# Kernel optimization log

Measured on AMD Instinct MI355X. Metric: run time of the kernel, lower is better.

Reference implementation:

```python
import jax, jax.numpy as jnp
import numpy as np
from jax import lax

V, D, L, H, MAXLEN = 32000, 512, 6, 8, 1024
DH = D // H
DFF = 4 * D
B, T = 8, 1024


def _ln(x, g, b, eps=1e-5):
    m = jnp.mean(x, axis=-1, keepdims=True)
    v = jnp.var(x, axis=-1, keepdims=True)
    return (x - m) * lax.rsqrt(v + eps) * g + b


def setup_inputs() -> dict:
    key = jax.random.key(0)
    ks = jax.random.split(key, 16)
    s = 0.02
    inp = {
        "idx": jax.random.randint(ks[0], (B, T), 0, V, dtype=jnp.int32),
        "wte": jax.random.normal(ks[1], (V, D), jnp.float32) * s,   # tied with head
        "wpe": jax.random.normal(ks[2], (MAXLEN, D), jnp.float32) * s,
        # per-layer stacked params [L, ...]
        "ln1_g": jnp.ones((L, D), jnp.float32),
        "ln1_b": jnp.zeros((L, D), jnp.float32),
        "w_qkv": jax.random.normal(ks[3], (L, D, 3 * D), jnp.float32) * s,
        "b_qkv": jnp.zeros((L, 3 * D), jnp.float32),
        "w_ao": jax.random.normal(ks[4], (L, D, D), jnp.float32) * s,
        "b_ao": jnp.zeros((L, D), jnp.float32),
        "ln2_g": jnp.ones((L, D), jnp.float32),
        "ln2_b": jnp.zeros((L, D), jnp.float32),
        "w_fc": jax.random.normal(ks[5], (L, D, DFF), jnp.float32) * s,
        "b_fc": jnp.zeros((L, DFF), jnp.float32),
        "w_pr": jax.random.normal(ks[6], (L, DFF, D), jnp.float32) * s,
        "b_pr": jnp.zeros((L, D), jnp.float32),
        "lnf_g": jnp.ones((D,), jnp.float32),
        "lnf_b": jnp.zeros((D,), jnp.float32),
    }
    return inp


def reference(idx, wte, wpe, ln1_g, ln1_b, w_qkv, b_qkv, w_ao, b_ao,
              ln2_g, ln2_b, w_fc, b_fc, w_pr, b_pr, lnf_g, lnf_b):
    Bx, Tx = idx.shape
    x = wte[idx] + wpe[:Tx]                      # [B,T,D]
    causal = jnp.tril(jnp.ones((Tx, Tx), bool))  # [T,T]
    scale = 1.0 / np.sqrt(DH)

    def block(x, p):
        (g1, b1, wqkv, bqkv, wao, bao, g2, b2, wfc, bfc, wpr, bpr) = p
        h = _ln(x, g1, b1)
        qkv = h @ wqkv + bqkv                    # [B,T,3D]
        q, k, v = jnp.split(qkv, 3, axis=-1)
        q = q.reshape(Bx, Tx, H, DH)
        k = k.reshape(Bx, Tx, H, DH)
        v = v.reshape(Bx, Tx, H, DH)
        att = jnp.einsum('bqhd,bkhd->bhqk', q, k) * scale
        att = jnp.where(causal, att, -jnp.inf)
        att = jax.nn.softmax(att, axis=-1)
        y = jnp.einsum('bhqk,bkhd->bqhd', att, v).reshape(Bx, Tx, D)
        x = x + y @ wao + bao
        h = _ln(x, g2, b2)
        h = jax.nn.gelu(h @ wfc + bfc, approximate=False)
        x = x + h @ wpr + bpr
        return x, None

    params = (ln1_g, ln1_b, w_qkv, b_qkv, w_ao, b_ao,
              ln2_g, ln2_b, w_fc, b_fc, w_pr, b_pr)
    x, _ = lax.scan(block, x, params)
    x = _ln(x, lnf_g, lnf_b)
    logits = x @ wte.T                           # tied head, [B,T,V]
    return logits
```

## Files before the change

### kernel.cpp

```cpp
#include <hip/hip_runtime.h>
#include <hip/hip_bf16.h>
#include <math.h>

#define V_   32000
#define D_   512
#define L_   6
#define H_   8
#define DH_  64
#define DFF_ 2048
#define B_   8
#define T_   1024
#define BT_  (B_*T_)

typedef __attribute__((ext_vector_type(4))) float f32x4;
typedef __attribute__((ext_vector_type(8))) short short8;
using bf16_t = __hip_bfloat16;

__device__ __forceinline__ float b2f(unsigned short u) {
    union { unsigned int i; float f; } v; v.i = ((unsigned int)u) << 16; return v.f;
}
__device__ __forceinline__ unsigned short f2b(float f) {
    bf16_t h = __float2bfloat16(f);
    return *reinterpret_cast<unsigned short*>(&h);
}
__device__ __forceinline__ void gl16(const void* g, void* l) {
    __builtin_amdgcn_global_load_lds((const __attribute__((address_space(1))) void*)g,
                                     (__attribute__((address_space(3))) void*)l, 16, 0, 0);
}
__device__ __forceinline__ float gelu_exact(float v) {
    return 0.5f * v * (1.0f + erff(v * 0.70710678118654752f));
}

__global__ __launch_bounds__(128) void embed_kernel(
        const int* __restrict__ idx, const float* __restrict__ wte,
        const float* __restrict__ wpe, float* __restrict__ x) {
    int bt = blockIdx.x;
    int t  = bt & (T_ - 1);
    int tok = idx[bt];
    const float4* wr = (const float4*)(wte + (size_t)tok * D_);
    const float4* pr = (const float4*)(wpe + (size_t)t * D_);
    float4* xr = (float4*)(x + (size_t)bt * D_);
    int i = threadIdx.x;
    float4 a = wr[i], b = pr[i];
    xr[i] = make_float4(a.x + b.x, a.y + b.y, a.z + b.z, a.w + b.w);
}

__global__ __launch_bounds__(128) void ln_kernel(
        const float* __restrict__ x, const float* __restrict__ g,
        const float* __restrict__ b, bf16_t* __restrict__ out) {
    int bt = blockIdx.x;
    int i  = threadIdx.x;
    float4 v = ((const float4*)(x + (size_t)bt * D_))[i];
    float s  = v.x + v.y + v.z + v.w;
    float sq = v.x*v.x + v.y*v.y + v.z*v.z + v.w*v.w;
    #pragma unroll
    for (int o = 32; o > 0; o >>= 1) {
        s  += __shfl_down(s,  o);
        sq += __shfl_down(sq, o);
    }
    __shared__ float ss[2], ssq[2];
    if ((i & 63) == 0) { ss[i >> 6] = s; ssq[i >> 6] = sq; }
    __syncthreads();
    float mean = (ss[0] + ss[1]) * (1.0f / D_);
    float var  = (ssq[0] + ssq[1]) * (1.0f / D_) - mean * mean;
    float rstd = rsqrtf(var + 1e-5f);
    float4 gg = ((const float4*)g)[i];
    float4 bb = ((const float4*)b)[i];
    ushort4 o4;
    o4.x = f2b((v.x - mean) * rstd * gg.x + bb.x);
    o4.y = f2b((v.y - mean) * rstd * gg.y + bb.y);
    o4.z = f2b((v.z - mean) * rstd * gg.z + bb.z);
    o4.w = f2b((v.w - mean) * rstd * gg.w + bb.w);
    ((ushort4*)(out + (size_t)bt * D_))[i] = o4;
}

__global__ __launch_bounds__(256) void conv_kernel(
        const float* __restrict__ s, bf16_t* __restrict__ d, int n4) {
    int i = blockIdx.x * 256 + threadIdx.x;
    if (i >= n4) return;
    float4 f = ((const float4*)s)[i];
    ushort4 u = make_ushort4(f2b(f.x), f2b(f.y), f2b(f.z), f2b(f.w));
    ((ushort4*)d)[i] = u;
}

__global__ __launch_bounds__(256) void tconv_kernel(
        const float* __restrict__ src, bf16_t* __restrict__ dst, int K, int N) {
    size_t ls = (size_t)K * N;
    const float* s = src + blockIdx.z * ls;
    bf16_t* d = dst + blockIdx.z * ls;
    __shared__ float tile[32][33];
    int n0 = blockIdx.x * 32, k0 = blockIdx.y * 32;
    int c = threadIdx.x & 31, r8 = threadIdx.x >> 5;
    #pragma unroll
    for (int i = 0; i < 4; ++i) {
        int r = r8 + i * 8;
        tile[r][c] = s[(size_t)(k0 + r) * N + n0 + c];
    }
    __syncthreads();
    #pragma unroll
    for (int i = 0; i < 4; ++i) {
        int r = r8 + i * 8;
        d[(size_t)(n0 + r) * K + k0 + c] = __float2bfloat16(tile[c][r]);
    }
}

template<int ACT, bool OBF, bool RES, bool CONVB>
__global__ __launch_bounds__(256) void mm_kernel(
        const bf16_t* __restrict__ A,
        const bf16_t* __restrict__ Bt,
        const float*  __restrict__ Bf,
        const float*  __restrict__ bias,
        const float*  __restrict__ res,
        void* __restrict__ Cout,
        int M, int N, int K)
{
    __shared__ __align__(16) unsigned short As[128 * 32];
    __shared__ __align__(16) unsigned short Bs[128 * 32];
    const int nwg = gridDim.x;
    const int orig = blockIdx.x;
    const int q8 = nwg >> 3, r8 = nwg & 7;
    const int xcd = orig & 7, lin = orig >> 3;
    const int wg = (xcd < r8) ? xcd * (q8 + 1) + lin
                              : r8 * (q8 + 1) + (xcd - r8) * q8 + lin;
    const int gym = M >> 7;
    const int by = wg % gym;
    const int bx = wg / gym;

    const int t    = threadIdx.x;
    const int row0 = by * 128;
    const int col0 = bx * 128;
    const int lane = t & 63;
    const int wid  = t >> 6;
    const int wm   = (wid & 1) * 64;
    const int wn   = (wid >> 1) * 64;
    const int fr   = lane & 15;
    const int fq   = lane >> 4;

    f32x4 acc[4][4];
    #pragma unroll
    for (int m = 0; m < 4; ++m)
        #pragma unroll
        for (int n = 0; n < 4; ++n)
            acc[m][n] = (f32x4)(0.0f);

    const unsigned short* Ab  = (const unsigned short*)A;
    const unsigned short* Btb = (const unsigned short*)Bt;

    for (int k0 = 0; k0 < K; k0 += 32) {
        __syncthreads();
        {
            int c = t;
            gl16(Ab + (size_t)(row0 + (c >> 2)) * K + k0 + (c & 3) * 8, As + c * 8);
            c = t + 256;
            gl16(Ab + (size_t)(row0 + (c >> 2)) * K + k0 + (c & 3) * 8, As + c * 8);
        }
        if (!CONVB) {
            int c = t;
            gl16(Btb + (size_t)(col0 + (c >> 2)) * K + k0 + (c & 3) * 8, Bs + c * 8);
            c = t + 256;
            gl16(Btb + (size_t)(col0 + (c >> 2)) * K + k0 + (c & 3) * 8, Bs + c * 8);
        } else {
            #pragma unroll
            for (int i = 0; i < 2; ++i) {
                int c = t + i * 256;
                const float* sp = Bf + (size_t)(col0 + (c >> 2)) * K + k0 + (c & 3) * 8;
                float4 f0 = ((const float4*)sp)[0];
                float4 f1 = ((const float4*)sp)[1];
                short8 pk;
                pk[0] = f2b(f0.x); pk[1] = f2b(f0.y); pk[2] = f2b(f0.z); pk[3] = f2b(f0.w);
                pk[4] = f2b(f1.x); pk[5] = f2b(f1.y); pk[6] = f2b(f1.z); pk[7] = f2b(f1.w);
                *(short8*)(Bs + (size_t)c * 8) = pk;
            }
        }
        __syncthreads();

        short8 av[4], bv[4];
        #pragma unroll
        for (int m = 0; m < 4; ++m)
            av[m] = *(const short8*)(As + (wm + m * 16 + fr) * 32 + fq * 8);
        #pragma unroll
        for (int n = 0; n < 4; ++n)
            bv[n] = *(const short8*)(Bs + (wn + n * 16 + fr) * 32 + fq * 8);
        #pragma unroll
        for (int m = 0; m < 4; ++m)
            #pragma unroll
            for (int n = 0; n < 4; ++n)
                acc[m][n] = __builtin_amdgcn_mfma_f32_16x16x32_bf16(av[m], bv[n], acc[m][n], 0, 0, 0);
    }

    #pragma unroll
    for (int n = 0; n < 4; ++n) {
        int col = col0 + wn + n * 16 + fr;
        float bb = bias ? bias[col] : 0.0f;
        #pragma unroll
        for (int m = 0; m < 4; ++m) {
            int rbase = row0 + wm + m * 16 + fq * 4;
            #pragma unroll
            for (int r = 0; r < 4; ++r) {
                float v = acc[m][n][r] + bb;
                if (ACT == 1) v = gelu_exact(v);
                size_t off = (size_t)(rbase + r) * N + col;
                if (RES) v += res[off];
                if (OBF) ((bf16_t*)Cout)[off] = __float2bfloat16(v);
                else     ((float*)Cout)[off]  = v;
            }
        }
    }
}

__global__ __launch_bounds__(256) void flash_kernel(
        const bf16_t* __restrict__ qkv, bf16_t* __restrict__ y)
{
    __shared__ __align__(16) unsigned short Ks[64][72];
    __shared__ __align__(16) unsigned short Vt[64][72];
    __shared__ __align__(16) unsigned short Pls[64][72];

    const int qt = blockIdx.x;
    const int bh = blockIdx.y;
    const int h  = bh & (H_ - 1);
    const int b  = bh >> 3;
    const int t  = threadIdx.x;
    const int lane = t & 63;
    const int w    = t >> 6;
    const int fr   = lane & 15;
    const int fq   = lane >> 4;

    const unsigned short* qkvb = (const unsigned short*)qkv;

    short8 avq[2];
    {
        const unsigned short* qrow = qkvb +
            (size_t)(b * T_ + qt * 64 + w * 16 + fr) * (3 * D_) + h * DH_;
        avq[0] = *(const short8*)(qrow + fq * 8);
        avq[1] = *(const short8*)(qrow + 32 + fq * 8);
    }

    float mi[4], li[4];
    f32x4 o[4];
    #pragma unroll
    for (int r = 0; r < 4; ++r) { mi[r] = -INFINITY; li[r] = 0.0f; o[r] = (f32x4)(0.0f); }
    f32x4 o2[4];
    #pragma unroll
    for (int r = 0; r < 4; ++r) o2[r] = (f32x4)(0.0f);
    f32x4 oacc[4];
    #pragma unroll
    for (int d = 0; d < 4; ++d) oacc[d] = (f32x4)(0.0f);
    (void)o; (void)o2;

    for (int jt = 0; jt <= qt; ++jt) {
        __syncthreads();
        {
            int j = t >> 2, seg = t & 3;
            const unsigned short* krow = qkvb +
                (size_t)(b * T_ + jt * 64 + j) * (3 * D_) + D_ + h * DH_ + seg * 16;
            *(short8*)&Ks[j][seg * 16]     = *(const short8*)(krow);
            *(short8*)&Ks[j][seg * 16 + 8] = *(const short8*)(krow + 8);
            const unsigned short* vrow = krow + D_;
            #pragma unroll
            for (int d4 = 0; d4 < 4; ++d4) {
                ushort4 u = *(const ushort4*)(vrow + d4 * 4);
                int d = seg * 16 + d4 * 4;
                Vt[d + 0][j] = u.x; Vt[d + 1][j] = u.y;
                Vt[d + 2][j] = u.z; Vt[d + 3][j] = u.w;
            }
        }
        __syncthreads();

        f32x4 s[4];
        #pragma unroll
        for (int jb = 0; jb < 4; ++jb) s[jb] = (f32x4)(0.0f);
        #pragma unroll
        for (int ks = 0; ks < 2; ++ks) {
            #pragma unroll
            for (int jb = 0; jb < 4; ++jb) {
                short8 bv = *(const short8*)(&Ks[jb * 16 + fr][ks * 32 + fq * 8]);
                s[jb] = __builtin_amdgcn_mfma_f32_16x16x32_bf16(avq[ks], bv, s[jb], 0, 0, 0);
            }
        }

        float sv[4][4];
        #pragma unroll
        for (int jb = 0; jb < 4; ++jb)
            #pragma unroll
            for (int r = 0; r < 4; ++r)
                sv[jb][r] = s[jb][r] * 0.125f;
        if (jt == qt) {
            #pragma unroll
            for (int jb = 0; jb < 4; ++jb) {
                int j_loc = jb * 16 + fr;
                #pragma unroll
                for (int r = 0; r < 4; ++r) {
                    int q_loc = w * 16 + fq * 4 + r;
                    if (jt * 64 + j_loc > qt * 64 + q_loc - w * 16 + w * 16) {}
                    if (j_loc > (fq * 4 + r) + (w * 16) - (w * 16) + (q_loc - q_loc)) {}
                }
            }
            #pragma unroll
            for (int jb = 0; jb < 4; ++jb) {
                int j_loc = jb * 16 + fr;
                #pragma unroll
                for (int r = 0; r < 4; ++r) {
                    int q_loc = w * 16 + fq * 4 + r;
                    if (j_loc > q_loc) sv[jb][r] = -INFINITY;
                }
            }
        }

        #pragma unroll
        for (int r = 0; r < 4; ++r) {
            float tm = fmaxf(fmaxf(sv[0][r], sv[1][r]), fmaxf(sv[2][r], sv[3][r]));
            tm = fmaxf(tm, __shfl_xor(tm, 1));
            tm = fmaxf(tm, __shfl_xor(tm, 2));
            tm = fmaxf(tm, __shfl_xor(tm, 4));
            tm = fmaxf(tm, __shfl_xor(tm, 8));
            float mnew = fmaxf(mi[r], tm);
            float corr = __expf(mi[r] - mnew);
            float tsum = 0.0f;
            #pragma unroll
            for (int jb = 0; jb < 4; ++jb) {
                float p = __expf(sv[jb][r] - mnew);
                sv[jb][r] = p;
                tsum += p;
            }
            tsum += __shfl_xor(tsum, 1);
            tsum += __shfl_xor(tsum, 2);
            tsum += __shfl_xor(tsum, 4);
            tsum += __shfl_xor(tsum, 8);
            li[r] = li[r] * corr + tsum;
            mi[r] = mnew;
            #pragma unroll
            for (int db = 0; db < 4; ++db) oacc[db][r] *= corr;
        }

        #pragma unroll
        for (int jb = 0; jb < 4; ++jb)
            #pragma unroll
            for (int r = 0; r < 4; ++r)
                Pls[w * 16 + fq * 4 + r][jb * 16 + fr] = f2b(sv[jb][r]);
        __syncthreads();

        #pragma unroll
        for (int ks = 0; ks < 2; ++ks) {
            short8 ap = *(const short8*)(&Pls[w * 16 + fr][ks * 32 + fq * 8]);
            #pragma unroll
            for (int db = 0; db < 4; ++db) {
                short8 bv = *(const short8*)(&Vt[db * 16 + fr][ks * 32 + fq * 8]);
                oacc[db] = __builtin_amdgcn_mfma_f32_16x16x32_bf16(ap, bv, oacc[db], 0, 0, 0);
            }
        }
    }

    unsigned short* yb = (unsigned short*)y;
    #pragma unroll
    for (int r = 0; r < 4; ++r) {
        float inv = 1.0f / li[r];
        size_t row = (size_t)(b * T_ + qt * 64 + w * 16 + fq * 4 + r);
        #pragma unroll
        for (int db = 0; db < 4; ++db)
            yb[row * D_ + h * DH_ + db * 16 + fr] = f2b(oacc[db][r] * inv);
    }
}

extern "C" void kernel_launch(void* const* d_in, const int* in_sizes, int n_in,
                              void* d_out, int out_size, void* d_ws, size_t ws_size,
                              hipStream_t stream) {
    const int*   idx   = (const int*)  d_in[0];
    const float* wte   = (const float*)d_in[1];
    const float* wpe   = (const float*)d_in[2];
    const float* ln1_g = (const float*)d_in[3];
    const float* ln1_b = (const float*)d_in[4];
    const float* w_qkv = (const float*)d_in[5];
    const float* b_qkv = (const float*)d_in[6];
    const float* w_ao  = (const float*)d_in[7];
    const float* b_ao  = (const float*)d_in[8];
    const float* ln2_g = (const float*)d_in[9];
    const float* ln2_b = (const float*)d_in[10];
    const float* w_fc  = (const float*)d_in[11];
    const float* b_fc  = (const float*)d_in[12];
    const float* w_pr  = (const float*)d_in[13];
    const float* b_pr  = (const float*)d_in[14];
    const float* lnf_g = (const float*)d_in[15];
    const float* lnf_b = (const float*)d_in[16];
    float* outf = (float*)d_out;

    char* base = (char*)d_out;
    size_t off = 0;
    auto alloc = [&](size_t bytes) {
        void* p = base + off;
        off += (bytes + 255) & ~(size_t)255;
        return p;
    };
    bf16_t* wqkvT = (bf16_t*)alloc((size_t)L_ * 3 * D_ * D_ * 2);
    bf16_t* waoT  = (bf16_t*)alloc((size_t)L_ * D_ * D_ * 2);
    bf16_t* wfcT  = (bf16_t*)alloc((size_t)L_ * DFF_ * D_ * 2);
    bf16_t* wprT  = (bf16_t*)alloc((size_t)L_ * D_ * DFF_ * 2);
    bf16_t* qkvb  = (bf16_t*)alloc((size_t)BT_ * 3 * D_ * 2);
    bf16_t* yb    = (bf16_t*)alloc((size_t)BT_ * D_ * 2);
    bf16_t* hab   = (bf16_t*)alloc((size_t)BT_ * D_ * 2);
    bf16_t* fcb   = (bf16_t*)alloc((size_t)BT_ * DFF_ * 2);
    float*  xb    = (float*) alloc((size_t)BT_ * D_ * 4);

    bf16_t* hfin = (bf16_t*)d_ws;
    size_t hbytes = ((size_t)BT_ * D_ * 2 + 255) & ~(size_t)255;
    bool wte_ws = ws_size >= hbytes + (size_t)V_ * D_ * 2 + 256;
    bf16_t* wteb = wte_ws ? (bf16_t*)((char*)d_ws + hbytes) : nullptr;

    if (wte_ws)
        conv_kernel<<<(V_ * D_ / 4 + 255) / 256, 256, 0, stream>>>(wte, wteb, V_ * D_ / 4);
    tconv_kernel<<<dim3(3 * D_ / 32, D_ / 32, L_), 256, 0, stream>>>(w_qkv, wqkvT, D_, 3 * D_);
    tconv_kernel<<<dim3(D_ / 32, D_ / 32, L_), 256, 0, stream>>>(w_ao, waoT, D_, D_);
    tconv_kernel<<<dim3(DFF_ / 32, D_ / 32, L_), 256, 0, stream>>>(w_fc, wfcT, D_, DFF_);
    tconv_kernel<<<dim3(D_ / 32, DFF_ / 32, L_), 256, 0, stream>>>(w_pr, wprT, DFF_, D_);

    embed_kernel<<<BT_, 128, 0, stream>>>(idx, wte, wpe, xb);

    for (int l = 0; l < L_; ++l) {
        ln_kernel<<<BT_, 128, 0, stream>>>(xb, ln1_g + l * D_, ln1_b + l * D_, hab);
        mm_kernel<0, true, false, false><<<12 * 64, 256, 0, stream>>>(
            hab, wqkvT + (size_t)l * 3 * D_ * D_, nullptr, b_qkv + (size_t)l * 3 * D_,
            nullptr, qkvb, BT_, 3 * D_, D_);
        flash_kernel<<<dim3(16, 64), 256, 0, stream>>>(qkvb, yb);
        mm_kernel<0, false, true, false><<<4 * 64, 256, 0, stream>>>(
            yb, waoT + (size_t)l * D_ * D_, nullptr, b_ao + (size_t)l * D_,
            xb, xb, BT_, D_, D_);
        ln_kernel<<<BT_, 128, 0, stream>>>(xb, ln2_g + l * D_, ln2_b + l * D_, hab);
        mm_kernel<1, true, false, false><<<16 * 64, 256, 0, stream>>>(
            hab, wfcT + (size_t)l * DFF_ * D_, nullptr, b_fc + (size_t)l * DFF_,
            nullptr, fcb, BT_, DFF_, D_);
        mm_kernel<0, false, true, false><<<4 * 64, 256, 0, stream>>>(
            fcb, wprT + (size_t)l * D_ * DFF_, nullptr, b_pr + (size_t)l * D_,
            xb, xb, BT_, D_, DFF_);
    }

    ln_kernel<<<BT_, 128, 0, stream>>>(xb, lnf_g, lnf_b, hfin);
    if (wte_ws)
        mm_kernel<0, false, false, false><<<250 * 64, 256, 0, stream>>>(
            hfin, wteb, nullptr, nullptr, nullptr, outf, BT_, V_, D_);
    else
        mm_kernel<0, false, false, true><<<250 * 64, 256, 0, stream>>>(
            hfin, nullptr, wte, nullptr, nullptr, outf, BT_, V_, D_);
}
```

Baseline: 2.012 ms.

## Double GEMM K-tile with XOR swizzle; enlarge flash query tile, reorder grid

The GEMM kernel now stages 64-wide K slices instead of 32, with an XOR swizzle on the LDS layout, which halves the number of barriers and is meant to reduce LDS bank conflicts. The flash attention kernel now handles 128 query rows per block with 512 threads and shares each K/V tile across 8 waves. It launches the heaviest query tiles first for better load balance and applies the causal mask on every tile. The barrier between writing and reading P is removed; this is safe only if each wave reads back just its own P rows, and the LDS footprint per block grows.

```diff
diff --git a/kernel.cpp b/kernel.cpp
--- a/kernel.cpp
+++ b/kernel.cpp
@@ -114,8 +114,8 @@
         void* __restrict__ Cout,
         int M, int N, int K)
 {
-    __shared__ __align__(16) unsigned short As[128 * 32];
-    __shared__ __align__(16) unsigned short Bs[128 * 32];
+    __shared__ __align__(16) unsigned short As[128 * 64];
+    __shared__ __align__(16) unsigned short Bs[128 * 64];
     const int nwg = gridDim.x;
     const int orig = blockIdx.x;
     const int q8 = nwg >> 3, r8 = nwg & 7;
@@ -146,24 +146,30 @@
     const unsigned short* Ab  = (const unsigned short*)A;
     const unsigned short* Btb = (const unsigned short*)Bt;
 
-    for (int k0 = 0; k0 < K; k0 += 32) {
+    for (int k0 = 0; k0 < K; k0 += 64) {
         __syncthreads();
-        {
-            int c = t;
-            gl16(Ab + (size_t)(row0 + (c >> 2)) * K + k0 + (c & 3) * 8, As + c * 8);
-            c = t + 256;
-            gl16(Ab + (size_t)(row0 + (c >> 2)) * K + k0 + (c & 3) * 8, As + c * 8);
+        #pragma unroll
+        for (int i = 0; i < 4; ++i) {
+            int c = t + i * 256;
+            int row = c >> 3;
+            int sl  = (c & 7) ^ (row & 7);
+            gl16(Ab + (size_t)(row0 + row) * K + k0 + sl * 8, As + (size_t)c * 8);
         }
         if (!CONVB) {
-            int c = t;
-            gl16(Btb + (size_t)(col0 + (c >> 2)) * K + k0 + (c & 3) * 8, Bs + c * 8);
-            c = t + 256;
-            gl16(Btb + (size_t)(col0 + (c >> 2)) * K + k0 + (c & 3) * 8, Bs + c * 8);
+            #pragma unroll
+            for (int i = 0; i < 4; ++i) {
+                int c = t + i * 256;
+                int row = c >> 3;
+                int sl  = (c & 7) ^ (row & 7);
+                gl16(Btb + (size_t)(col0 + row) * K + k0 + sl * 8, Bs + (size_t)c * 8);
+            }
         } else {
             #pragma unroll
-            for (int i = 0; i < 2; ++i) {
+            for (int i = 0; i < 4; ++i) {
                 int c = t + i * 256;
-                const float* sp = Bf + (size_t)(col0 + (c >> 2)) * K + k0 + (c & 3) * 8;
+                int row = c >> 3;
+                int sl  = (c & 7) ^ (row & 7);
+                const float* sp = Bf + (size_t)(col0 + row) * K + k0 + sl * 8;
                 float4 f0 = ((const float4*)sp)[0];
                 float4 f1 = ((const float4*)sp)[1];
                 short8 pk;
@@ -174,18 +180,27 @@
         }
         __syncthreads();
 
-        short8 av[4], bv[4];
-        #pragma unroll
-        for (int m = 0; m < 4; ++m)
-            av[m] = *(const short8*)(As + (wm + m * 16 + fr) * 32 + fq * 8);
-        #pragma unroll
-        for (int n = 0; n < 4; ++n)
-            bv[n] = *(const short8*)(Bs + (wn + n * 16 + fr) * 32 + fq * 8);
-        #pragma unroll
-        for (int m = 0; m < 4; ++m)
-            #pragma unroll
-            for (int n = 0; n < 4; ++n)
-                acc[m][n] = __builtin_amdgcn_mfma_f32_16x16x32_bf16(av[m], bv[n], acc[m][n], 0, 0, 0);
+        #pragma unroll
+        for (int kk = 0; kk < 2; ++kk) {
+            short8 av[4], bv[4];
+            #pragma unroll
+            for (int m = 0; m < 4; ++m) {
+                int R = wm + m * 16 + fr;
+                int sl = (kk * 4 + fq) ^ (fr & 7);
+                av[m] = *(const short8*)(As + (size_t)R * 64 + sl * 8);
+            }
+            #pragma unroll
+            for (int n = 0; n < 4; ++n) {
+                int R = wn + n * 16 + fr;
+                int sl = (kk * 4 + fq) ^ (fr & 7);
+                bv[n] = *(const short8*)(Bs + (size_t)R * 64 + sl * 8);
+            }
+            #pragma unroll
+            for (int m = 0; m < 4; ++m)
+                #pragma unroll
+                for (int n = 0; n < 4; ++n)
+                    acc[m][n] = __builtin_amdgcn_mfma_f32_16x16x32_bf16(av[m], bv[n], acc[m][n], 0, 0, 0);
+        }
     }
 
     #pragma unroll
@@ -208,15 +223,15 @@
     }
 }
 
-__global__ __launch_bounds__(256) void flash_kernel(
+__global__ __launch_bounds__(512, 2) void flash_kernel(
         const bf16_t* __restrict__ qkv, bf16_t* __restrict__ y)
 {
     __shared__ __align__(16) unsigned short Ks[64][72];
     __shared__ __align__(16) unsigned short Vt[64][72];
-    __shared__ __align__(16) unsigned short Pls[64][72];
-
-    const int qt = blockIdx.x;
-    const int bh = blockIdx.y;
+    __shared__ __align__(16) unsigned short Pls[128][72];
+
+    const int qt = (T_ / 128 - 1) - (blockIdx.x >> 6);
+    const int bh = blockIdx.x & 63;
     const int h  = bh & (H_ - 1);
     const int b  = bh >> 3;
     const int t  = threadIdx.x;
@@ -230,39 +245,32 @@
     short8 avq[2];
     {
         const unsigned short* qrow = qkvb +
-            (size_t)(b * T_ + qt * 64 + w * 16 + fr) * (3 * D_) + h * DH_;
+            (size_t)(b * T_ + qt * 128 + w * 16 + fr) * (3 * D_) + h * DH_;
         avq[0] = *(const short8*)(qrow + fq * 8);
         avq[1] = *(const short8*)(qrow + 32 + fq * 8);
     }
 
     float mi[4], li[4];
-    f32x4 o[4];
-    #pragma unroll
-    for (int r = 0; r < 4; ++r) { mi[r] = -INFINITY; li[r] = 0.0f; o[r] = (f32x4)(0.0f); }
-    f32x4 o2[4];
-    #pragma unroll
-    for (int r = 0; r < 4; ++r) o2[r] = (f32x4)(0.0f);
     f32x4 oacc[4];
     #pragma unroll
+    for (int r = 0; r < 4; ++r) { mi[r] = -INFINITY; li[r] = 0.0f; }
+    #pragma unroll
     for (int d = 0; d < 4; ++d) oacc[d] = (f32x4)(0.0f);
-    (void)o; (void)o2;
-
-    for (int jt = 0; jt <= qt; ++jt) {
+
+    const int nt = 2 * qt + 2;
+    for (int jt = 0; jt < nt; ++jt) {
         __syncthreads();
         {
-            int j = t >> 2, seg = t & 3;
-            const unsigned short* krow = qkvb +
-                (size_t)(b * T_ + jt * 64 + j) * (3 * D_) + D_ + h * DH_ + seg * 16;
-            *(short8*)&Ks[j][seg * 16]     = *(const short8*)(krow);
-            *(short8*)&Ks[j][seg * 16 + 8] = *(const short8*)(krow + 8);
-            const unsigned short* vrow = krow + D_;
-            #pragma unroll
-            for (int d4 = 0; d4 < 4; ++d4) {
-                ushort4 u = *(const ushort4*)(vrow + d4 * 4);
-                int d = seg * 16 + d4 * 4;
-                Vt[d + 0][j] = u.x; Vt[d + 1][j] = u.y;
-                Vt[d + 2][j] = u.z; Vt[d + 3][j] = u.w;
-            }
+            int j = t >> 3, seg = t & 7;
+            const unsigned short* kr = qkvb +
+                (size_t)(b * T_ + jt * 64 + j) * (3 * D_) + D_ + h * DH_ + seg * 8;
+            *(short8*)&Ks[j][seg * 8] = *(const short8*)kr;
+            short8 vv = *(const short8*)(kr + D_);
+            int dbase = seg * 8;
+            Vt[dbase + 0][j] = vv[0]; Vt[dbase + 1][j] = vv[1];
+            Vt[dbase + 2][j] = vv[2]; Vt[dbase + 3][j] = vv[3];
+            Vt[dbase + 4][j] = vv[4]; Vt[dbase + 5][j] = vv[5];
+            Vt[dbase + 6][j] = vv[6]; Vt[dbase + 7][j] = vv[7];
         }
         __syncthreads();
 
@@ -279,30 +287,14 @@
         }
 
         float sv[4][4];
-        #pragma unroll
-        for (int jb = 0; jb < 4; ++jb)
-            #pragma unroll
-            for (int r = 0; r < 4; ++r)
-                sv[jb][r] = s[jb][r] * 0.125f;
-        if (jt == qt) {
-            #pragma unroll
-            for (int jb = 0; jb < 4; ++jb) {
-                int j_loc = jb * 16 + fr;
-                #pragma unroll
-                for (int r = 0; r < 4; ++r) {
-                    int q_loc = w * 16 + fq * 4 + r;
-                    if (jt * 64 + j_loc > qt * 64 + q_loc - w * 16 + w * 16) {}
-                    if (j_loc > (fq * 4 + r) + (w * 16) - (w * 16) + (q_loc - q_loc)) {}
-                }
-            }
-            #pragma unroll
-            for (int jb = 0; jb < 4; ++jb) {
-                int j_loc = jb * 16 + fr;
-                #pragma unroll
-                for (int r = 0; r < 4; ++r) {
-                    int q_loc = w * 16 + fq * 4 + r;
-                    if (j_loc > q_loc) sv[jb][r] = -INFINITY;
-                }
+        const int qgb = qt * 128 + w * 16 + fq * 4;
+        #pragma unroll
+        for (int jb = 0; jb < 4; ++jb) {
+            int jg = jt * 64 + jb * 16 + fr;
+            #pragma unroll
+            for (int r = 0; r < 4; ++r) {
+                float x = s[jb][r] * 0.125f;
+                sv[jb][r] = (jg > qgb + r) ? -INFINITY : x;
             }
         }
 
@@ -337,7 +329,6 @@
             #pragma unroll
             for (int r = 0; r < 4; ++r)
                 Pls[w * 16 + fq * 4 + r][jb * 16 + fr] = f2b(sv[jb][r]);
-        __syncthreads();
 
         #pragma unroll
         for (int ks = 0; ks < 2; ++ks) {
@@ -354,7 +345,7 @@
     #pragma unroll
     for (int r = 0; r < 4; ++r) {
         float inv = 1.0f / li[r];
-        size_t row = (size_t)(b * T_ + qt * 64 + w * 16 + fq * 4 + r);
+        size_t row = (size_t)(b * T_ + qt * 128 + w * 16 + fq * 4 + r);
         #pragma unroll
         for (int db = 0; db < 4; ++db)
             yb[row * D_ + h * DH_ + db * 16 + fr] = f2b(oacc[db][r] * inv);
@@ -419,7 +410,7 @@
         mm_kernel<0, true, false, false><<<12 * 64, 256, 0, stream>>>(
             hab, wqkvT + (size_t)l * 3 * D_ * D_, nullptr, b_qkv + (size_t)l * 3 * D_,
             nullptr, qkvb, BT_, 3 * D_, D_);
-        flash_kernel<<<dim3(16, 64), 256, 0, stream>>>(qkvb, yb);
+        flash_kernel<<<512, 512, 0, stream>>>(qkvb, yb);
         mm_kernel<0, false, true, false><<<4 * 64, 256, 0, stream>>>(
             yb, waoT + (size_t)l * D_ * D_, nullptr, b_ao + (size_t)l * D_,
             xb, xb, BT_, D_, D_);
```

Result: faster. 1.797 ms (-10.7%).
